# Performance work log

Hardware: AMD Instinct MI355X
Metric: run time of the kernel (lower is better)

The kernel has to match this reference:

```python
import jax, jax.numpy as jnp
import numpy as np

N_NODES = 100000
N_EDGES = 1600000
IN_CH = 128
HID = 32
N_GRAPHS = 64


def _gcn_conv(x, src, dst, W, b, n_nodes):
    # PyG GCNConv defaults: x' = D^{-1/2} (A + I) D^{-1/2} (x W) + b
    h = x @ W                                   # [N, out]
    loop = jnp.arange(n_nodes, dtype=src.dtype)
    s = jnp.concatenate([src, loop])            # add self-loops
    d = jnp.concatenate([dst, loop])
    deg = jax.ops.segment_sum(jnp.ones_like(d, dtype=h.dtype), d, num_segments=n_nodes)
    dinv = jnp.where(deg > 0, jax.lax.rsqrt(deg), 0.0)
    norm = dinv[s] * dinv[d]                    # [E+N]
    msg = h[s] * norm[:, None]                  # gather + scale
    out = jax.ops.segment_sum(msg, d, num_segments=n_nodes)  # scatter-add
    return out + b


def setup_inputs() -> dict:
    key = jax.random.key(0)
    ks = jax.random.split(key, 8)
    x = jax.random.normal(ks[0], (N_NODES, IN_CH), dtype=jnp.float32)
    edge_index = jax.random.randint(ks[1], (2, N_EDGES), 0, N_NODES, dtype=jnp.int32)
    batch = jnp.sort(jax.random.randint(ks[2], (N_NODES,), 0, N_GRAPHS, dtype=jnp.int32))
    W1 = jax.random.normal(ks[3], (IN_CH, HID), dtype=jnp.float32) * (1.0 / np.sqrt(IN_CH))
    b1 = jnp.zeros((HID,), dtype=jnp.float32)
    W2 = jax.random.normal(ks[4], (HID, HID), dtype=jnp.float32) * (1.0 / np.sqrt(HID))
    b2 = jnp.zeros((HID,), dtype=jnp.float32)
    Ws = jax.random.normal(ks[5], (HID, HID), dtype=jnp.float32) * (1.0 / np.sqrt(HID))
    bs = jnp.zeros((HID,), dtype=jnp.float32)
    return {"x": x, "edge_index": edge_index, "batch": batch,
            "W1": W1, "b1": b1, "W2": W2, "b2": b2, "Ws": Ws, "bs": bs}


def reference(x, edge_index, batch, W1, b1, W2, b2, Ws, bs):
    src, dst = edge_index[0], edge_index[1]
    n = x.shape[0]
    h = _gcn_conv(x, src, dst, W1, b1, n)
    h = jax.nn.relu(h)
    h = _gcn_conv(h, src, dst, W2, b2, n)       # [N, HID] node embeddings
    # global_mean_pool over graph ids
    ones = jnp.ones((n,), dtype=h.dtype)
    cnt = jax.ops.segment_sum(ones, batch, num_segments=N_GRAPHS)
    gsum = jax.ops.segment_sum(h, batch, num_segments=N_GRAPHS)
    g = gsum / jnp.maximum(cnt, 1.0)[:, None]   # [G, HID]
    summary = g @ Ws + bs
    return summary, h
```

## Files before the change

### kernel.cpp

```cpp
#include <hip/hip_runtime.h>

#define N_NODES  100000
#define N_EDGES  1600000
#define IN_CH    128
#define HID      32
#define N_GRAPHS 64

#define NBIN   391
#define CHUNK  4096
#define MGRID  391
#define STG    5120

#define OFF_B      0
#define OFF_EDGEPK 3200000
#define OFF_CSR    4800000
#define OFF_COLT   6400000
#define OFF_BINB   6400391
#define OFF_ROWPTR 6400784
#define OFF_DINV   6500785

__device__ __forceinline__ unsigned bfr(float f) {
    unsigned u = __float_as_uint(f);
    u += 0x7fffu + ((u >> 16) & 1u);
    return u >> 16;
}
__device__ __forceinline__ float bflo(unsigned w) { return __uint_as_float(w << 16); }
__device__ __forceinline__ float bfhi(unsigned w) { return __uint_as_float(w & 0xffff0000u); }

__global__ __launch_bounds__(512) void hist_kernel(const int* __restrict__ dst,
                                                   int* __restrict__ H) {
    __shared__ int s[512];
    int t = threadIdx.x, wg = blockIdx.x;
    s[t] = 0;
    __syncthreads();
    int e0 = wg * CHUNK, e1 = min(e0 + CHUNK, N_EDGES);
    for (int e = e0 + t; e < e1; e += 512) {
        int d = dst[e];
        if ((unsigned)d < N_NODES) atomicAdd(&s[d >> 8], 1);
    }
    __syncthreads();
    if (t < NBIN) H[t * MGRID + wg] = s[t];
}

__global__ __launch_bounds__(512) void scanrow_kernel(int* __restrict__ H,
                                                      int* __restrict__ colT) {
    __shared__ int s[512];
    int t = threadIdx.x, bin = blockIdx.x;
    s[t] = (t < MGRID) ? H[bin * MGRID + t] : 0;
    __syncthreads();
    for (int off = 1; off < 512; off <<= 1) {
        int v = (t >= off) ? s[t - off] : 0;
        __syncthreads();
        if (t >= off) s[t] += v;
        __syncthreads();
    }
    if (t < MGRID) H[bin * MGRID + t] = t ? s[t - 1] : 0;
    if (t == 0) colT[bin] = s[MGRID - 1];
}

__global__ __launch_bounds__(512) void scanbase_kernel(const int* __restrict__ colT,
                                                       int* __restrict__ binB,
                                                       int* __restrict__ row_ptr) {
    __shared__ int s[512];
    int t = threadIdx.x;
    s[t] = (t < NBIN) ? colT[t] : 0;
    __syncthreads();
    for (int off = 1; off < 512; off <<= 1) {
        int v = (t >= off) ? s[t - off] : 0;
        __syncthreads();
        if (t >= off) s[t] += v;
        __syncthreads();
    }
    if (t < NBIN) binB[t] = t ? s[t - 1] : 0;
    if (t == 0) { binB[NBIN] = s[NBIN - 1]; row_ptr[N_NODES] = s[NBIN - 1]; }
}

__global__ __launch_bounds__(512) void msplit_kernel(const int* __restrict__ src,
                                                     const int* __restrict__ dst,
                                                     const int* __restrict__ H,
                                                     const int* __restrict__ binB,
                                                     int* __restrict__ edgepk) {
    __shared__ int s[512];
    __shared__ int cur[NBIN];
    __shared__ int gb[NBIN];
    __shared__ int stage[CHUNK];
    __shared__ int gof[CHUNK];
    int t = threadIdx.x, wg = blockIdx.x;
    s[t] = 0;
    __syncthreads();
    int e0 = wg * CHUNK, e1 = min(e0 + CHUNK, N_EDGES);
    for (int e = e0 + t; e < e1; e += 512) {
        int d = dst[e];
        if ((unsigned)d < N_NODES) atomicAdd(&s[d >> 8], 1);
    }
    __syncthreads();
    for (int off = 1; off < 512; off <<= 1) {
        int v = (t >= off) ? s[t - off] : 0;
        __syncthreads();
        if (t >= off) s[t] += v;
        __syncthreads();
    }
    if (t < NBIN) {
        int lo = t ? s[t - 1] : 0;
        cur[t] = lo;
        gb[t] = binB[t] + H[t * MGRID + wg] - lo;
    }
    __syncthreads();
    for (int e = e0 + t; e < e1; e += 512) {
        int d = dst[e];
        if ((unsigned)d < N_NODES) {
            int b = d >> 8;
            int p = atomicAdd(&cur[b], 1);
            stage[p] = (src[e] << 8) | (d & 255);
            gof[p] = gb[b];
        }
    }
    __syncthreads();
    int total = s[511];
    for (int p = t; p < total; p += 512)
        edgepk[gof[p] + p] = stage[p];
}

__global__ __launch_bounds__(256) void csr2_kernel(const int* __restrict__ edgepk,
                                                   const int* __restrict__ binB,
                                                   int* __restrict__ row_ptr,
                                                   float* __restrict__ dinv,
                                                   int* __restrict__ csr) {
    __shared__ int cnt[256], s[256], cur[256];
    __shared__ int stage[STG];
    int t = threadIdx.x, bin = blockIdx.x;
    int ebase = binB[bin], eend = binB[bin + 1];
    int n = eend - ebase;
    cnt[t] = 0;
    __syncthreads();
    for (int p = ebase + t; p < eend; p += 256)
        atomicAdd(&cnt[edgepk[p] & 255], 1);
    __syncthreads();
    s[t] = cnt[t];
    __syncthreads();
    for (int off = 1; off < 256; off <<= 1) {
        int v = (t >= off) ? s[t - off] : 0;
        __syncthreads();
        if (t >= off) s[t] += v;
        __syncthreads();
    }
    int excl = t ? s[t - 1] : 0;
    int node = (bin << 8) + t;
    if (node < N_NODES) {
        dinv[node] = rsqrtf((float)(cnt[t] + 1));
        row_ptr[node] = ebase + excl;
    }
    cur[t] = excl;
    __syncthreads();
    for (int p = ebase + t; p < eend; p += 256) {
        int w = edgepk[p];
        int l = atomicAdd(&cur[w & 255], 1);
        int sv = w >> 8;
        if (l < STG) stage[l] = sv;
        else csr[ebase + l] = sv;
    }
    __syncthreads();
    int lim = min(n, STG);
    for (int l = t; l < lim; l += 256)
        csr[ebase + l] = stage[l];
}

#define XS1 132
__global__ __launch_bounds__(256) void gemm1_kernel(const float* __restrict__ x,
                                                    const float* __restrict__ W1,
                                                    const float* __restrict__ dinv,
                                                    unsigned* __restrict__ Bu) {
    __shared__ float Wl[IN_CH * HID];
    __shared__ float xs[32 * XS1];
    int tid = threadIdx.x;
    for (int j = tid; j < IN_CH * HID / 4; j += 256)
        ((float4*)Wl)[j] = ((const float4*)W1)[j];
    int row0 = blockIdx.x * 32;
    const float4* x4 = (const float4*)(x + (size_t)row0 * IN_CH);
    for (int j = tid; j < 32 * IN_CH / 4; j += 256) {
        int r = j >> 5, k4 = j & 31;
        ((float4*)&xs[r * XS1])[k4] = x4[j];
    }
    __syncthreads();
    int r = tid >> 3, cg = (tid & 7) * 4;
    const float* xr = &xs[r * XS1];
    float4 acc = {0.f, 0.f, 0.f, 0.f};
    #pragma unroll 8
    for (int k = 0; k < IN_CH; ++k) {
        float xv = xr[k];
        float4 w = *(const float4*)&Wl[k * HID + cg];
        acc.x += xv * w.x; acc.y += xv * w.y; acc.z += xv * w.z; acc.w += xv * w.w;
    }
    int row = row0 + r;
    float dv = dinv[row];
    uint2 p;
    p.x = bfr(acc.x * dv) | (bfr(acc.y * dv) << 16);
    p.y = bfr(acc.z * dv) | (bfr(acc.w * dv) << 16);
    *(uint2*)&Bu[(size_t)row * 16 + (tid & 7) * 2] = p;
}

#define XS2 36
__global__ __launch_bounds__(256) void gemm2_kernel(const float* __restrict__ in,
                                                    const float* __restrict__ W2,
                                                    const float* __restrict__ dinv,
                                                    unsigned* __restrict__ Bu) {
    __shared__ float Wl[HID * HID];
    __shared__ float xs[32 * XS2];
    int tid = threadIdx.x;
    ((float4*)Wl)[tid] = ((const float4*)W2)[tid];
    int row0 = blockIdx.x * 32;
    const float4* in4 = (const float4*)(in + (size_t)row0 * HID);
    {
        int r = tid >> 3, k4 = tid & 7;
        ((float4*)&xs[r * XS2])[k4] = in4[tid];
    }
    __syncthreads();
    int r = tid >> 3, cg = (tid & 7) * 4;
    const float* xr = &xs[r * XS2];
    float4 acc = {0.f, 0.f, 0.f, 0.f};
    #pragma unroll
    for (int k = 0; k < HID; ++k) {
        float xv = xr[k];
        float4 w = *(const float4*)&Wl[k * HID + cg];
        acc.x += xv * w.x; acc.y += xv * w.y; acc.z += xv * w.z; acc.w += xv * w.w;
    }
    int row = row0 + r;
    float dv = dinv[row];
    uint2 p;
    p.x = bfr(acc.x * dv) | (bfr(acc.y * dv) << 16);
    p.y = bfr(acc.z * dv) | (bfr(acc.w * dv) << 16);
    *(uint2*)&Bu[(size_t)row * 16 + (tid & 7) * 2] = p;
}

__global__ __launch_bounds__(256) void layer_kernel(const unsigned* __restrict__ Bu,
                                                    const int* __restrict__ csr,
                                                    const int* __restrict__ row_ptr,
                                                    const float* __restrict__ dinv,
                                                    const float* __restrict__ bias,
                                                    float* __restrict__ out,
                                                    int relu) {
    int tid = threadIdx.x;
    int node = blockIdx.x * 16 + (tid >> 4);
    int c2 = tid & 15;
    unsigned ws = Bu[(size_t)node * 16 + c2];
    float a0 = bflo(ws), a1 = bfhi(ws);
    int j = row_ptr[node], re = row_ptr[node + 1];
    for (; j + 8 <= re; j += 8) {
        int s0 = csr[j + 0], s1 = csr[j + 1], s2 = csr[j + 2], s3 = csr[j + 3];
        int s4 = csr[j + 4], s5 = csr[j + 5], s6 = csr[j + 6], s7 = csr[j + 7];
        unsigned w0 = Bu[(size_t)s0 * 16 + c2], w1 = Bu[(size_t)s1 * 16 + c2];
        unsigned w2 = Bu[(size_t)s2 * 16 + c2], w3 = Bu[(size_t)s3 * 16 + c2];
        unsigned w4 = Bu[(size_t)s4 * 16 + c2], w5 = Bu[(size_t)s5 * 16 + c2];
        unsigned w6 = Bu[(size_t)s6 * 16 + c2], w7 = Bu[(size_t)s7 * 16 + c2];
        a0 += ((bflo(w0) + bflo(w1)) + (bflo(w2) + bflo(w3)))
            + ((bflo(w4) + bflo(w5)) + (bflo(w6) + bflo(w7)));
        a1 += ((bfhi(w0) + bfhi(w1)) + (bfhi(w2) + bfhi(w3)))
            + ((bfhi(w4) + bfhi(w5)) + (bfhi(w6) + bfhi(w7)));
    }
    if (j + 4 <= re) {
        int s0 = csr[j], s1 = csr[j + 1], s2 = csr[j + 2], s3 = csr[j + 3];
        unsigned w0 = Bu[(size_t)s0 * 16 + c2], w1 = Bu[(size_t)s1 * 16 + c2];
        unsigned w2 = Bu[(size_t)s2 * 16 + c2], w3 = Bu[(size_t)s3 * 16 + c2];
        a0 += (bflo(w0) + bflo(w1)) + (bflo(w2) + bflo(w3));
        a1 += (bfhi(w0) + bfhi(w1)) + (bfhi(w2) + bfhi(w3));
        j += 4;
    }
    for (; j < re; ++j) {
        unsigned w = Bu[(size_t)csr[j] * 16 + c2];
        a0 += bflo(w); a1 += bfhi(w);
    }
    float dv = dinv[node];
    float2 o;
    o.x = a0 * dv + bias[2 * c2];
    o.y = a1 * dv + bias[2 * c2 + 1];
    if (relu) { o.x = fmaxf(o.x, 0.f); o.y = fmaxf(o.y, 0.f); }
    *(float2*)&out[(size_t)node * HID + 2 * c2] = o;
}

__global__ __launch_bounds__(256) void pool_kernel(const float* __restrict__ h,
                                                   const int* __restrict__ batch,
                                                   float* __restrict__ gsum,
                                                   float* __restrict__ cnt) {
    __shared__ float pool[N_GRAPHS * HID];
    __shared__ float cntl[N_GRAPHS];
    __shared__ int gmin, gmax;
    int t = threadIdx.x;
    for (int j = t; j < N_GRAPHS * HID; j += 256) pool[j] = 0.f;
    if (t < N_GRAPHS) cntl[t] = 0.f;
    if (t == 0) { gmin = N_GRAPHS; gmax = -1; }
    __syncthreads();
    int start = blockIdx.x * 256;
    int end = min(start + 256, N_NODES);
    int c = t & 31;
    float racc = 0.f;
    int rg = -1, rcnt = 0;
    for (int nb = start + (t >> 5); nb < end; nb += 8) {
        float v = h[(size_t)nb * HID + c];
        int g = batch[nb];
        if (g != rg) {
            if ((unsigned)rg < N_GRAPHS) {
                atomicAdd(&pool[rg * HID + c], racc);
                if (c == 0) {
                    atomicAdd(&cntl[rg], (float)rcnt);
                    atomicMin(&gmin, rg); atomicMax(&gmax, rg);
                }
            }
            rg = g; racc = v; rcnt = 1;
        } else { racc += v; ++rcnt; }
    }
    if ((unsigned)rg < N_GRAPHS) {
        atomicAdd(&pool[rg * HID + c], racc);
        if (c == 0) {
            atomicAdd(&cntl[rg], (float)rcnt);
            atomicMin(&gmin, rg); atomicMax(&gmax, rg);
        }
    }
    __syncthreads();
    int lo = gmin, hi = gmax;
    if (hi >= lo) {
        int span = (hi - lo + 1) * HID;
        for (int j = t; j < span; j += 256)
            atomicAdd(&gsum[lo * HID + j], pool[lo * HID + j]);
        for (int j = t; j <= hi - lo; j += 256)
            atomicAdd(&cnt[lo + j], cntl[lo + j]);
    }
}

__global__ void summary_kernel(const float* __restrict__ gsum, const float* __restrict__ cnt,
                               const float* __restrict__ Ws, const float* __restrict__ bs,
                               float* __restrict__ out) {
    int g = blockIdx.x, c = threadIdx.x;
    float inv = 1.f / fmaxf(cnt[g], 1.f);
    float acc = bs[c];
    #pragma unroll
    for (int k = 0; k < HID; ++k)
        acc += gsum[g * HID + k] * inv * Ws[k * HID + c];
    out[g * HID + c] = acc;
}

extern "C" void kernel_launch(void* const* d_in, const int* in_sizes, int n_in,
                              void* d_out, int out_size, void* d_ws, size_t ws_size,
                              hipStream_t stream) {
    const float* x    = (const float*)d_in[0];
    const int* edge   = (const int*)d_in[1];
    const int* src    = edge;
    const int* dst    = edge + N_EDGES;
    const int* batch  = (const int*)d_in[2];
    const float* W1   = (const float*)d_in[3];
    const float* b1   = (const float*)d_in[4];
    const float* W2   = (const float*)d_in[5];
    const float* b2   = (const float*)d_in[6];
    const float* Ws   = (const float*)d_in[7];
    const float* bs   = (const float*)d_in[8];

    float* ws      = (float*)d_ws;
    unsigned* Bu   = (unsigned*)(ws + OFF_B);
    int*   H       = (int*)(ws + OFF_B);
    int*   edgepk  = (int*)(ws + OFF_EDGEPK);
    int*   csr     = (int*)(ws + OFF_CSR);
    int*   colT    = (int*)(ws + OFF_COLT);
    int*   binB    = (int*)(ws + OFF_BINB);
    int*   row_ptr = (int*)(ws + OFF_ROWPTR);
    float* dinv    = ws + OFF_DINV;
    float* gsum    = ws + OFF_EDGEPK;
    float* cnt     = gsum + N_GRAPHS * HID;

    float* out     = (float*)d_out;
    float* out_sum = out;
    float* out_h   = out + N_GRAPHS * HID;

    hist_kernel    <<<MGRID, 512, 0, stream>>>(dst, H);
    scanrow_kernel <<<NBIN,  512, 0, stream>>>(H, colT);
    scanbase_kernel<<<1,     512, 0, stream>>>(colT, binB, row_ptr);
    msplit_kernel  <<<MGRID, 512, 0, stream>>>(src, dst, H, binB, edgepk);
    csr2_kernel    <<<NBIN,  256, 0, stream>>>(edgepk, binB, row_ptr, dinv, csr);

    gemm1_kernel<<<N_NODES / 32, 256, 0, stream>>>(x, W1, dinv, Bu);
    layer_kernel<<<N_NODES / 16, 256, 0, stream>>>(Bu, csr, row_ptr, dinv, b1, out_h, 1);

    gemm2_kernel<<<N_NODES / 32, 256, 0, stream>>>(out_h, W2, dinv, Bu);
    layer_kernel<<<N_NODES / 16, 256, 0, stream>>>(Bu, csr, row_ptr, dinv, b2, out_h, 0);

    hipMemsetAsync(gsum, 0, (N_GRAPHS * HID + N_GRAPHS) * sizeof(float), stream);
    pool_kernel<<<NBIN, 256, 0, stream>>>(out_h, batch, gsum, cnt);
    summary_kernel<<<N_GRAPHS, HID, 0, stream>>>(gsum, cnt, Ws, bs, out_sum);
}
```

Measured before the change: 240.2 us.

## Fuse layer-1 aggregation with W2 GEMM and layer-2 aggregation with mean pooling

The first aggregation kernel now applies bias and ReLU, stages each node's hidden row in shared memory, and multiplies by W2 in place. It writes the bf16 pre-scaled features for layer 2 directly, so the float hidden activations no longer go through global memory. The second aggregation kernel accumulates per-graph sums and counts into shared memory and flushes them with global atomics, which removes the separate pool pass over the output. In exchange there are more block-level syncs, many more small global atomic flushes (one per 16-node block), and a second bf16 buffer that reuses the edgepk workspace region.

```diff
diff --git a/kernel.cpp b/kernel.cpp
--- a/kernel.cpp
+++ b/kernel.cpp
@@ -18,6 +18,7 @@
 #define OFF_BINB   6400391
 #define OFF_ROWPTR 6400784
 #define OFF_DINV   6500785
+#define OFF_GS     6600800
 
 __device__ __forceinline__ unsigned bfr(float f) {
     unsigned u = __float_as_uint(f);
@@ -199,51 +200,21 @@
     *(uint2*)&Bu[(size_t)row * 16 + (tid & 7) * 2] = p;
 }
 
-#define XS2 36
-__global__ __launch_bounds__(256) void gemm2_kernel(const float* __restrict__ in,
-                                                    const float* __restrict__ W2,
-                                                    const float* __restrict__ dinv,
-                                                    unsigned* __restrict__ Bu) {
-    __shared__ float Wl[HID * HID];
-    __shared__ float xs[32 * XS2];
+__global__ __launch_bounds__(256) void layer1_fused_kernel(const unsigned* __restrict__ Bu,
+                                                           const int* __restrict__ csr,
+                                                           const int* __restrict__ row_ptr,
+                                                           const float* __restrict__ dinv,
+                                                           const float* __restrict__ bias,
+                                                           const float* __restrict__ W2,
+                                                           unsigned* __restrict__ Bu2) {
+    __shared__ float W2l[HID * HID];
+    __shared__ float hs[16 * 33];
     int tid = threadIdx.x;
-    ((float4*)Wl)[tid] = ((const float4*)W2)[tid];
-    int row0 = blockIdx.x * 32;
-    const float4* in4 = (const float4*)(in + (size_t)row0 * HID);
-    {
-        int r = tid >> 3, k4 = tid & 7;
-        ((float4*)&xs[r * XS2])[k4] = in4[tid];
-    }
-    __syncthreads();
-    int r = tid >> 3, cg = (tid & 7) * 4;
-    const float* xr = &xs[r * XS2];
-    float4 acc = {0.f, 0.f, 0.f, 0.f};
-    #pragma unroll
-    for (int k = 0; k < HID; ++k) {
-        float xv = xr[k];
-        float4 w = *(const float4*)&Wl[k * HID + cg];
-        acc.x += xv * w.x; acc.y += xv * w.y; acc.z += xv * w.z; acc.w += xv * w.w;
-    }
-    int row = row0 + r;
-    float dv = dinv[row];
-    uint2 p;
-    p.x = bfr(acc.x * dv) | (bfr(acc.y * dv) << 16);
-    p.y = bfr(acc.z * dv) | (bfr(acc.w * dv) << 16);
-    *(uint2*)&Bu[(size_t)row * 16 + (tid & 7) * 2] = p;
-}
-
-__global__ __launch_bounds__(256) void layer_kernel(const unsigned* __restrict__ Bu,
-                                                    const int* __restrict__ csr,
-                                                    const int* __restrict__ row_ptr,
-                                                    const float* __restrict__ dinv,
-                                                    const float* __restrict__ bias,
-                                                    float* __restrict__ out,
-                                                    int relu) {
-    int tid = threadIdx.x;
+    ((float4*)W2l)[tid] = ((const float4*)W2)[tid];
     int node = blockIdx.x * 16 + (tid >> 4);
     int c2 = tid & 15;
-    unsigned ws = Bu[(size_t)node * 16 + c2];
-    float a0 = bflo(ws), a1 = bfhi(ws);
+    unsigned ws0 = Bu[(size_t)node * 16 + c2];
+    float a0 = bflo(ws0), a1 = bfhi(ws0);
     int j = row_ptr[node], re = row_ptr[node + 1];
     for (; j + 8 <= re; j += 8) {
         int s0 = csr[j + 0], s1 = csr[j + 1], s2 = csr[j + 2], s3 = csr[j + 3];
@@ -270,60 +241,83 @@
         a0 += bflo(w); a1 += bfhi(w);
     }
     float dv = dinv[node];
+    float h0 = fmaxf(a0 * dv + bias[2 * c2], 0.f);
+    float h1 = fmaxf(a1 * dv + bias[2 * c2 + 1], 0.f);
+    int r = tid >> 4;
+    hs[r * 33 + 2 * c2]     = h0;
+    hs[r * 33 + 2 * c2 + 1] = h1;
+    __syncthreads();
+    const float* hr = &hs[r * 33];
+    float o0 = 0.f, o1 = 0.f;
+    #pragma unroll
+    for (int k = 0; k < HID; ++k) {
+        float hv = hr[k];
+        float2 w = *(const float2*)&W2l[k * HID + 2 * c2];
+        o0 += hv * w.x; o1 += hv * w.y;
+    }
+    Bu2[(size_t)node * 16 + c2] = bfr(o0 * dv) | (bfr(o1 * dv) << 16);
+}
+
+__global__ __launch_bounds__(256) void layer2_pool_kernel(const unsigned* __restrict__ Bu,
+                                                          const int* __restrict__ csr,
+                                                          const int* __restrict__ row_ptr,
+                                                          const float* __restrict__ dinv,
+                                                          const float* __restrict__ bias,
+                                                          const int* __restrict__ batch,
+                                                          float* __restrict__ out,
+                                                          float* __restrict__ gsum,
+                                                          float* __restrict__ cnt) {
+    __shared__ float pl[N_GRAPHS * HID];
+    __shared__ float pc[N_GRAPHS];
+    int tid = threadIdx.x;
+    int node0 = blockIdx.x * 16;
+    int g0 = batch[node0];
+    int span = batch[node0 + 15] - g0 + 1;
+    for (int q = tid; q < span * HID; q += 256) pl[q] = 0.f;
+    if (tid < span) pc[tid] = 0.f;
+    int node = node0 + (tid >> 4);
+    int c2 = tid & 15;
+    unsigned ws0 = Bu[(size_t)node * 16 + c2];
+    float a0 = bflo(ws0), a1 = bfhi(ws0);
+    int j = row_ptr[node], re = row_ptr[node + 1];
+    for (; j + 8 <= re; j += 8) {
+        int s0 = csr[j + 0], s1 = csr[j + 1], s2 = csr[j + 2], s3 = csr[j + 3];
+        int s4 = csr[j + 4], s5 = csr[j + 5], s6 = csr[j + 6], s7 = csr[j + 7];
+        unsigned w0 = Bu[(size_t)s0 * 16 + c2], w1 = Bu[(size_t)s1 * 16 + c2];
+        unsigned w2 = Bu[(size_t)s2 * 16 + c2], w3 = Bu[(size_t)s3 * 16 + c2];
+        unsigned w4 = Bu[(size_t)s4 * 16 + c2], w5 = Bu[(size_t)s5 * 16 + c2];
+        unsigned w6 = Bu[(size_t)s6 * 16 + c2], w7 = Bu[(size_t)s7 * 16 + c2];
+        a0 += ((bflo(w0) + bflo(w1)) + (bflo(w2) + bflo(w3)))
+            + ((bflo(w4) + bflo(w5)) + (bflo(w6) + bflo(w7)));
+        a1 += ((bfhi(w0) + bfhi(w1)) + (bfhi(w2) + bfhi(w3)))
+            + ((bfhi(w4) + bfhi(w5)) + (bfhi(w6) + bfhi(w7)));
+    }
+    if (j + 4 <= re) {
+        int s0 = csr[j], s1 = csr[j + 1], s2 = csr[j + 2], s3 = csr[j + 3];
+        unsigned w0 = Bu[(size_t)s0 * 16 + c2], w1 = Bu[(size_t)s1 * 16 + c2];
+        unsigned w2 = Bu[(size_t)s2 * 16 + c2], w3 = Bu[(size_t)s3 * 16 + c2];
+        a0 += (bflo(w0) + bflo(w1)) + (bflo(w2) + bflo(w3));
+        a1 += (bfhi(w0) + bfhi(w1)) + (bfhi(w2) + bfhi(w3));
+        j += 4;
+    }
+    for (; j < re; ++j) {
+        unsigned w = Bu[(size_t)csr[j] * 16 + c2];
+        a0 += bflo(w); a1 += bfhi(w);
+    }
+    float dv = dinv[node];
     float2 o;
     o.x = a0 * dv + bias[2 * c2];
     o.y = a1 * dv + bias[2 * c2 + 1];
-    if (relu) { o.x = fmaxf(o.x, 0.f); o.y = fmaxf(o.y, 0.f); }
     *(float2*)&out[(size_t)node * HID + 2 * c2] = o;
-}
-
-__global__ __launch_bounds__(256) void pool_kernel(const float* __restrict__ h,
-                                                   const int* __restrict__ batch,
-                                                   float* __restrict__ gsum,
-                                                   float* __restrict__ cnt) {
-    __shared__ float pool[N_GRAPHS * HID];
-    __shared__ float cntl[N_GRAPHS];
-    __shared__ int gmin, gmax;
-    int t = threadIdx.x;
-    for (int j = t; j < N_GRAPHS * HID; j += 256) pool[j] = 0.f;
-    if (t < N_GRAPHS) cntl[t] = 0.f;
-    if (t == 0) { gmin = N_GRAPHS; gmax = -1; }
-    __syncthreads();
-    int start = blockIdx.x * 256;
-    int end = min(start + 256, N_NODES);
-    int c = t & 31;
-    float racc = 0.f;
-    int rg = -1, rcnt = 0;
-    for (int nb = start + (t >> 5); nb < end; nb += 8) {
-        float v = h[(size_t)nb * HID + c];
-        int g = batch[nb];
-        if (g != rg) {
-            if ((unsigned)rg < N_GRAPHS) {
-                atomicAdd(&pool[rg * HID + c], racc);
-                if (c == 0) {
-                    atomicAdd(&cntl[rg], (float)rcnt);
-                    atomicMin(&gmin, rg); atomicMax(&gmax, rg);
-                }
-            }
-            rg = g; racc = v; rcnt = 1;
-        } else { racc += v; ++rcnt; }
-    }
-    if ((unsigned)rg < N_GRAPHS) {
-        atomicAdd(&pool[rg * HID + c], racc);
-        if (c == 0) {
-            atomicAdd(&cntl[rg], (float)rcnt);
-            atomicMin(&gmin, rg); atomicMax(&gmax, rg);
-        }
-    }
-    __syncthreads();
-    int lo = gmin, hi = gmax;
-    if (hi >= lo) {
-        int span = (hi - lo + 1) * HID;
-        for (int j = t; j < span; j += 256)
-            atomicAdd(&gsum[lo * HID + j], pool[lo * HID + j]);
-        for (int j = t; j <= hi - lo; j += 256)
-            atomicAdd(&cnt[lo + j], cntl[lo + j]);
-    }
+    int gl = batch[node] - g0;
+    __syncthreads();
+    atomicAdd(&pl[gl * HID + 2 * c2], o.x);
+    atomicAdd(&pl[gl * HID + 2 * c2 + 1], o.y);
+    if (c2 == 0) atomicAdd(&pc[gl], 1.f);
+    __syncthreads();
+    for (int q = tid; q < span * HID; q += 256)
+        atomicAdd(&gsum[g0 * HID + q], pl[q]);
+    if (tid < span) atomicAdd(&cnt[g0 + tid], pc[tid]);
 }
 
 __global__ void summary_kernel(const float* __restrict__ gsum, const float* __restrict__ cnt,
@@ -354,7 +348,8 @@
     const float* bs   = (const float*)d_in[8];
 
     float* ws      = (float*)d_ws;
-    unsigned* Bu   = (unsigned*)(ws + OFF_B);
+    unsigned* Bu1  = (unsigned*)(ws + OFF_B);
+    unsigned* Bu2  = (unsigned*)(ws + OFF_EDGEPK);
     int*   H       = (int*)(ws + OFF_B);
     int*   edgepk  = (int*)(ws + OFF_EDGEPK);
     int*   csr     = (int*)(ws + OFF_CSR);
@@ -362,7 +357,7 @@
     int*   binB    = (int*)(ws + OFF_BINB);
     int*   row_ptr = (int*)(ws + OFF_ROWPTR);
     float* dinv    = ws + OFF_DINV;
-    float* gsum    = ws + OFF_EDGEPK;
+    float* gsum    = ws + OFF_GS;
     float* cnt     = gsum + N_GRAPHS * HID;
 
     float* out     = (float*)d_out;
@@ -375,13 +370,11 @@
     msplit_kernel  <<<MGRID, 512, 0, stream>>>(src, dst, H, binB, edgepk);
     csr2_kernel    <<<NBIN,  256, 0, stream>>>(edgepk, binB, row_ptr, dinv, csr);
 
-    gemm1_kernel<<<N_NODES / 32, 256, 0, stream>>>(x, W1, dinv, Bu);
-    layer_kernel<<<N_NODES / 16, 256, 0, stream>>>(Bu, csr, row_ptr, dinv, b1, out_h, 1);
-
-    gemm2_kernel<<<N_NODES / 32, 256, 0, stream>>>(out_h, W2, dinv, Bu);
-    layer_kernel<<<N_NODES / 16, 256, 0, stream>>>(Bu, csr, row_ptr, dinv, b2, out_h, 0);
-
+    gemm1_kernel<<<N_NODES / 32, 256, 0, stream>>>(x, W1, dinv, Bu1);
     hipMemsetAsync(gsum, 0, (N_GRAPHS * HID + N_GRAPHS) * sizeof(float), stream);
-    pool_kernel<<<NBIN, 256, 0, stream>>>(out_h, batch, gsum, cnt);
+    layer1_fused_kernel<<<N_NODES / 16, 256, 0, stream>>>(Bu1, csr, row_ptr, dinv, b1, W2, Bu2);
+
+    layer2_pool_kernel<<<N_NODES / 16, 256, 0, stream>>>(Bu2, csr, row_ptr, dinv, b2, batch,
+                                                         out_h, gsum, cnt);
     summary_kernel<<<N_GRAPHS, HID, 0, stream>>>(gsum, cnt, Ws, bs, out_sum);
 }
```

Measured after the change: 267.1 us. +11.2%, slower.

## Split bf16 feature table into two column planes and gather each half separately

Applied to the files above, without the earlier changes.

The bf16 message table is stored as two 16-channel planes of 800k words each, and each layer's aggregation runs as two passes, one per plane. Each pass gathers 32-byte rows from a 3.2 MB plane instead of 64-byte rows from a 6.4 MB table, so the working set is more likely to stay cache-resident. CSR index loads and output stores become nontemporal, and the second layer's table moves to a separate workspace region. In exchange the CSR indices and row pointers are read twice per layer and there are two extra kernel launches.

```diff
diff --git a/kernel.cpp b/kernel.cpp
--- a/kernel.cpp
+++ b/kernel.cpp
@@ -10,6 +10,7 @@
 #define CHUNK  4096
 #define MGRID  391
 #define STG    5120
+#define PLN    800000
 
 #define OFF_B      0
 #define OFF_EDGEPK 3200000
@@ -18,6 +19,9 @@
 #define OFF_BINB   6400391
 #define OFF_ROWPTR 6400784
 #define OFF_DINV   6500785
+#define OFF_GS     6600800
+
+typedef float v2f __attribute__((ext_vector_type(2)));
 
 __device__ __forceinline__ unsigned bfr(float f) {
     unsigned u = __float_as_uint(f);
@@ -196,7 +200,8 @@
     uint2 p;
     p.x = bfr(acc.x * dv) | (bfr(acc.y * dv) << 16);
     p.y = bfr(acc.z * dv) | (bfr(acc.w * dv) << 16);
-    *(uint2*)&Bu[(size_t)row * 16 + (tid & 7) * 2] = p;
+    int c8 = tid & 7;
+    *(uint2*)(Bu + (size_t)(c8 >> 2) * PLN + (size_t)row * 8 + (c8 & 3) * 2) = p;
 }
 
 #define XS2 36
@@ -229,52 +234,62 @@
     uint2 p;
     p.x = bfr(acc.x * dv) | (bfr(acc.y * dv) << 16);
     p.y = bfr(acc.z * dv) | (bfr(acc.w * dv) << 16);
-    *(uint2*)&Bu[(size_t)row * 16 + (tid & 7) * 2] = p;
-}
-
-__global__ __launch_bounds__(256) void layer_kernel(const unsigned* __restrict__ Bu,
-                                                    const int* __restrict__ csr,
-                                                    const int* __restrict__ row_ptr,
-                                                    const float* __restrict__ dinv,
-                                                    const float* __restrict__ bias,
-                                                    float* __restrict__ out,
-                                                    int relu) {
+    int c8 = tid & 7;
+    *(uint2*)(Bu + (size_t)(c8 >> 2) * PLN + (size_t)row * 8 + (c8 & 3) * 2) = p;
+}
+
+__global__ __launch_bounds__(256) void gather_kernel(const unsigned* __restrict__ Bp,
+                                                     const int* __restrict__ csr,
+                                                     const int* __restrict__ row_ptr,
+                                                     const float* __restrict__ dinv,
+                                                     const float* __restrict__ bias,
+                                                     float* __restrict__ outp,
+                                                     int relu) {
     int tid = threadIdx.x;
-    int node = blockIdx.x * 16 + (tid >> 4);
-    int c2 = tid & 15;
-    unsigned ws = Bu[(size_t)node * 16 + c2];
-    float a0 = bflo(ws), a1 = bfhi(ws);
+    int node = blockIdx.x * 32 + (tid >> 3);
+    int c = tid & 7;
+    unsigned ws0 = Bp[(size_t)node * 8 + c];
+    float a0 = bflo(ws0), a1 = bfhi(ws0);
     int j = row_ptr[node], re = row_ptr[node + 1];
     for (; j + 8 <= re; j += 8) {
-        int s0 = csr[j + 0], s1 = csr[j + 1], s2 = csr[j + 2], s3 = csr[j + 3];
-        int s4 = csr[j + 4], s5 = csr[j + 5], s6 = csr[j + 6], s7 = csr[j + 7];
-        unsigned w0 = Bu[(size_t)s0 * 16 + c2], w1 = Bu[(size_t)s1 * 16 + c2];
-        unsigned w2 = Bu[(size_t)s2 * 16 + c2], w3 = Bu[(size_t)s3 * 16 + c2];
-        unsigned w4 = Bu[(size_t)s4 * 16 + c2], w5 = Bu[(size_t)s5 * 16 + c2];
-        unsigned w6 = Bu[(size_t)s6 * 16 + c2], w7 = Bu[(size_t)s7 * 16 + c2];
+        int s0 = __builtin_nontemporal_load(csr + j + 0);
+        int s1 = __builtin_nontemporal_load(csr + j + 1);
+        int s2 = __builtin_nontemporal_load(csr + j + 2);
+        int s3 = __builtin_nontemporal_load(csr + j + 3);
+        int s4 = __builtin_nontemporal_load(csr + j + 4);
+        int s5 = __builtin_nontemporal_load(csr + j + 5);
+        int s6 = __builtin_nontemporal_load(csr + j + 6);
+        int s7 = __builtin_nontemporal_load(csr + j + 7);
+        unsigned w0 = Bp[(size_t)s0 * 8 + c], w1 = Bp[(size_t)s1 * 8 + c];
+        unsigned w2 = Bp[(size_t)s2 * 8 + c], w3 = Bp[(size_t)s3 * 8 + c];
+        unsigned w4 = Bp[(size_t)s4 * 8 + c], w5 = Bp[(size_t)s5 * 8 + c];
+        unsigned w6 = Bp[(size_t)s6 * 8 + c], w7 = Bp[(size_t)s7 * 8 + c];
         a0 += ((bflo(w0) + bflo(w1)) + (bflo(w2) + bflo(w3)))
             + ((bflo(w4) + bflo(w5)) + (bflo(w6) + bflo(w7)));
         a1 += ((bfhi(w0) + bfhi(w1)) + (bfhi(w2) + bfhi(w3)))
             + ((bfhi(w4) + bfhi(w5)) + (bfhi(w6) + bfhi(w7)));
     }
     if (j + 4 <= re) {
-        int s0 = csr[j], s1 = csr[j + 1], s2 = csr[j + 2], s3 = csr[j + 3];
-        unsigned w0 = Bu[(size_t)s0 * 16 + c2], w1 = Bu[(size_t)s1 * 16 + c2];
-        unsigned w2 = Bu[(size_t)s2 * 16 + c2], w3 = Bu[(size_t)s3 * 16 + c2];
+        int s0 = __builtin_nontemporal_load(csr + j + 0);
+        int s1 = __builtin_nontemporal_load(csr + j + 1);
+        int s2 = __builtin_nontemporal_load(csr + j + 2);
+        int s3 = __builtin_nontemporal_load(csr + j + 3);
+        unsigned w0 = Bp[(size_t)s0 * 8 + c], w1 = Bp[(size_t)s1 * 8 + c];
+        unsigned w2 = Bp[(size_t)s2 * 8 + c], w3 = Bp[(size_t)s3 * 8 + c];
         a0 += (bflo(w0) + bflo(w1)) + (bflo(w2) + bflo(w3));
         a1 += (bfhi(w0) + bfhi(w1)) + (bfhi(w2) + bfhi(w3));
         j += 4;
     }
     for (; j < re; ++j) {
-        unsigned w = Bu[(size_t)csr[j] * 16 + c2];
+        unsigned w = Bp[(size_t)__builtin_nontemporal_load(csr + j) * 8 + c];
         a0 += bflo(w); a1 += bfhi(w);
     }
     float dv = dinv[node];
-    float2 o;
-    o.x = a0 * dv + bias[2 * c2];
-    o.y = a1 * dv + bias[2 * c2 + 1];
+    v2f o;
+    o.x = a0 * dv + bias[2 * c];
+    o.y = a1 * dv + bias[2 * c + 1];
     if (relu) { o.x = fmaxf(o.x, 0.f); o.y = fmaxf(o.y, 0.f); }
-    *(float2*)&out[(size_t)node * HID + 2 * c2] = o;
+    __builtin_nontemporal_store(o, (v2f*)(outp + (size_t)node * HID + 2 * c));
 }
 
 __global__ __launch_bounds__(256) void pool_kernel(const float* __restrict__ h,
@@ -354,7 +369,8 @@
     const float* bs   = (const float*)d_in[8];
 
     float* ws      = (float*)d_ws;
-    unsigned* Bu   = (unsigned*)(ws + OFF_B);
+    unsigned* Bu1  = (unsigned*)(ws + OFF_B);
+    unsigned* Bu2  = (unsigned*)(ws + OFF_EDGEPK);
     int*   H       = (int*)(ws + OFF_B);
     int*   edgepk  = (int*)(ws + OFF_EDGEPK);
     int*   csr     = (int*)(ws + OFF_CSR);
@@ -362,7 +378,7 @@
     int*   binB    = (int*)(ws + OFF_BINB);
     int*   row_ptr = (int*)(ws + OFF_ROWPTR);
     float* dinv    = ws + OFF_DINV;
-    float* gsum    = ws + OFF_EDGEPK;
+    float* gsum    = ws + OFF_GS;
     float* cnt     = gsum + N_GRAPHS * HID;
 
     float* out     = (float*)d_out;
@@ -375,11 +391,13 @@
     msplit_kernel  <<<MGRID, 512, 0, stream>>>(src, dst, H, binB, edgepk);
     csr2_kernel    <<<NBIN,  256, 0, stream>>>(edgepk, binB, row_ptr, dinv, csr);
 
-    gemm1_kernel<<<N_NODES / 32, 256, 0, stream>>>(x, W1, dinv, Bu);
-    layer_kernel<<<N_NODES / 16, 256, 0, stream>>>(Bu, csr, row_ptr, dinv, b1, out_h, 1);
-
-    gemm2_kernel<<<N_NODES / 32, 256, 0, stream>>>(out_h, W2, dinv, Bu);
-    layer_kernel<<<N_NODES / 16, 256, 0, stream>>>(Bu, csr, row_ptr, dinv, b2, out_h, 0);
+    gemm1_kernel<<<N_NODES / 32, 256, 0, stream>>>(x, W1, dinv, Bu1);
+    gather_kernel<<<N_NODES / 32, 256, 0, stream>>>(Bu1,       csr, row_ptr, dinv, b1,      out_h,      1);
+    gather_kernel<<<N_NODES / 32, 256, 0, stream>>>(Bu1 + PLN, csr, row_ptr, dinv, b1 + 16, out_h + 16, 1);
+
+    gemm2_kernel<<<N_NODES / 32, 256, 0, stream>>>(out_h, W2, dinv, Bu2);
+    gather_kernel<<<N_NODES / 32, 256, 0, stream>>>(Bu2,       csr, row_ptr, dinv, b2,      out_h,      0);
+    gather_kernel<<<N_NODES / 32, 256, 0, stream>>>(Bu2 + PLN, csr, row_ptr, dinv, b2 + 16, out_h + 16, 0);
 
     hipMemsetAsync(gsum, 0, (N_GRAPHS * HID + N_GRAPHS) * sizeof(float), stream);
     pool_kernel<<<NBIN, 256, 0, stream>>>(out_h, batch, gsum, cnt);
```

Measured after the change: 275.6 us. 14.7% more time.

## Balance edge aggregation across threads with LDS atomic accumulation per node group

Applied to the files above, without the earlier changes.

The CSR build now packs each edge's local destination index into the top byte alongside the source id. The aggregation kernel splits a block's contiguous 32-node edge range evenly across 16 thread groups and accumulates into shared memory with atomics, then adds the self-loop term, scales, and writes float4 outputs. The aim is to remove load imbalance from varying node degrees, at the cost of many LDS atomic adds per edge. Packing 24-bit source ids limits the node count to 2^24.

```diff
diff --git a/kernel.cpp b/kernel.cpp
--- a/kernel.cpp
+++ b/kernel.cpp
@@ -10,6 +10,7 @@
 #define CHUNK  4096
 #define MGRID  391
 #define STG    5120
+#define GN     32
 
 #define OFF_B      0
 #define OFF_EDGEPK 3200000
@@ -154,10 +155,11 @@
     __syncthreads();
     for (int p = ebase + t; p < eend; p += 256) {
         int w = edgepk[p];
-        int l = atomicAdd(&cur[w & 255], 1);
-        int sv = w >> 8;
-        if (l < STG) stage[l] = sv;
-        else csr[ebase + l] = sv;
+        int dl = w & 255;
+        int l = atomicAdd(&cur[dl], 1);
+        int pk = (int)(((unsigned)dl << 24) | (unsigned)(w >> 8));
+        if (l < STG) stage[l] = pk;
+        else csr[ebase + l] = pk;
     }
     __syncthreads();
     int lim = min(n, STG);
@@ -232,49 +234,83 @@
     *(uint2*)&Bu[(size_t)row * 16 + (tid & 7) * 2] = p;
 }
 
-__global__ __launch_bounds__(256) void layer_kernel(const unsigned* __restrict__ Bu,
-                                                    const int* __restrict__ csr,
-                                                    const int* __restrict__ row_ptr,
-                                                    const float* __restrict__ dinv,
-                                                    const float* __restrict__ bias,
-                                                    float* __restrict__ out,
-                                                    int relu) {
+#define AS 33
+__global__ __launch_bounds__(256) void gather_acc_kernel(const unsigned* __restrict__ Bu,
+                                                         const int* __restrict__ csr,
+                                                         const int* __restrict__ row_ptr,
+                                                         const float* __restrict__ dinv,
+                                                         const float* __restrict__ bias,
+                                                         float* __restrict__ out,
+                                                         int relu) {
+    __shared__ float acc[GN * AS];
     int tid = threadIdx.x;
-    int node = blockIdx.x * 16 + (tid >> 4);
-    int c2 = tid & 15;
-    unsigned ws = Bu[(size_t)node * 16 + c2];
-    float a0 = bflo(ws), a1 = bfhi(ws);
-    int j = row_ptr[node], re = row_ptr[node + 1];
-    for (; j + 8 <= re; j += 8) {
-        int s0 = csr[j + 0], s1 = csr[j + 1], s2 = csr[j + 2], s3 = csr[j + 3];
-        int s4 = csr[j + 4], s5 = csr[j + 5], s6 = csr[j + 6], s7 = csr[j + 7];
-        unsigned w0 = Bu[(size_t)s0 * 16 + c2], w1 = Bu[(size_t)s1 * 16 + c2];
-        unsigned w2 = Bu[(size_t)s2 * 16 + c2], w3 = Bu[(size_t)s3 * 16 + c2];
-        unsigned w4 = Bu[(size_t)s4 * 16 + c2], w5 = Bu[(size_t)s5 * 16 + c2];
-        unsigned w6 = Bu[(size_t)s6 * 16 + c2], w7 = Bu[(size_t)s7 * 16 + c2];
-        a0 += ((bflo(w0) + bflo(w1)) + (bflo(w2) + bflo(w3)))
-            + ((bflo(w4) + bflo(w5)) + (bflo(w6) + bflo(w7)));
-        a1 += ((bfhi(w0) + bfhi(w1)) + (bfhi(w2) + bfhi(w3)))
-            + ((bfhi(w4) + bfhi(w5)) + (bfhi(w6) + bfhi(w7)));
-    }
-    if (j + 4 <= re) {
-        int s0 = csr[j], s1 = csr[j + 1], s2 = csr[j + 2], s3 = csr[j + 3];
-        unsigned w0 = Bu[(size_t)s0 * 16 + c2], w1 = Bu[(size_t)s1 * 16 + c2];
-        unsigned w2 = Bu[(size_t)s2 * 16 + c2], w3 = Bu[(size_t)s3 * 16 + c2];
-        a0 += (bflo(w0) + bflo(w1)) + (bflo(w2) + bflo(w3));
-        a1 += (bfhi(w0) + bfhi(w1)) + (bfhi(w2) + bfhi(w3));
-        j += 4;
-    }
-    for (; j < re; ++j) {
-        unsigned w = Bu[(size_t)csr[j] * 16 + c2];
-        a0 += bflo(w); a1 += bfhi(w);
-    }
+    int n0 = blockIdx.x * GN;
+    for (int q = tid; q < GN * AS; q += 256) acc[q] = 0.f;
+    int j0 = row_ptr[n0], j1 = row_ptr[n0 + GN];
+    __syncthreads();
+    int g = tid >> 4, c2 = tid & 15;
+    int lbase = n0 & 255;
+    int nE = j1 - j0;
+    int epg = (nE + 15) >> 4;
+    int e = j0 + g * epg;
+    int ee = min(e + epg, j1);
+    for (; e + 8 <= ee; e += 8) {
+        unsigned u0 = (unsigned)csr[e + 0], u1 = (unsigned)csr[e + 1];
+        unsigned u2 = (unsigned)csr[e + 2], u3 = (unsigned)csr[e + 3];
+        unsigned u4 = (unsigned)csr[e + 4], u5 = (unsigned)csr[e + 5];
+        unsigned u6 = (unsigned)csr[e + 6], u7 = (unsigned)csr[e + 7];
+        unsigned w0 = Bu[(size_t)(u0 & 0xFFFFFFu) * 16 + c2];
+        unsigned w1 = Bu[(size_t)(u1 & 0xFFFFFFu) * 16 + c2];
+        unsigned w2 = Bu[(size_t)(u2 & 0xFFFFFFu) * 16 + c2];
+        unsigned w3 = Bu[(size_t)(u3 & 0xFFFFFFu) * 16 + c2];
+        unsigned w4 = Bu[(size_t)(u4 & 0xFFFFFFu) * 16 + c2];
+        unsigned w5 = Bu[(size_t)(u5 & 0xFFFFFFu) * 16 + c2];
+        unsigned w6 = Bu[(size_t)(u6 & 0xFFFFFFu) * 16 + c2];
+        unsigned w7 = Bu[(size_t)(u7 & 0xFFFFFFu) * 16 + c2];
+        int d0 = (int)(u0 >> 24) - lbase, d1 = (int)(u1 >> 24) - lbase;
+        int d2 = (int)(u2 >> 24) - lbase, d3 = (int)(u3 >> 24) - lbase;
+        int d4 = (int)(u4 >> 24) - lbase, d5 = (int)(u5 >> 24) - lbase;
+        int d6 = (int)(u6 >> 24) - lbase, d7 = (int)(u7 >> 24) - lbase;
+        atomicAdd(&acc[d0 * AS + 2 * c2],     bflo(w0));
+        atomicAdd(&acc[d0 * AS + 2 * c2 + 1], bfhi(w0));
+        atomicAdd(&acc[d1 * AS + 2 * c2],     bflo(w1));
+        atomicAdd(&acc[d1 * AS + 2 * c2 + 1], bfhi(w1));
+        atomicAdd(&acc[d2 * AS + 2 * c2],     bflo(w2));
+        atomicAdd(&acc[d2 * AS + 2 * c2 + 1], bfhi(w2));
+        atomicAdd(&acc[d3 * AS + 2 * c2],     bflo(w3));
+        atomicAdd(&acc[d3 * AS + 2 * c2 + 1], bfhi(w3));
+        atomicAdd(&acc[d4 * AS + 2 * c2],     bflo(w4));
+        atomicAdd(&acc[d4 * AS + 2 * c2 + 1], bfhi(w4));
+        atomicAdd(&acc[d5 * AS + 2 * c2],     bflo(w5));
+        atomicAdd(&acc[d5 * AS + 2 * c2 + 1], bfhi(w5));
+        atomicAdd(&acc[d6 * AS + 2 * c2],     bflo(w6));
+        atomicAdd(&acc[d6 * AS + 2 * c2 + 1], bfhi(w6));
+        atomicAdd(&acc[d7 * AS + 2 * c2],     bflo(w7));
+        atomicAdd(&acc[d7 * AS + 2 * c2 + 1], bfhi(w7));
+    }
+    for (; e < ee; ++e) {
+        unsigned u = (unsigned)csr[e];
+        unsigned w = Bu[(size_t)(u & 0xFFFFFFu) * 16 + c2];
+        int d = (int)(u >> 24) - lbase;
+        atomicAdd(&acc[d * AS + 2 * c2],     bflo(w));
+        atomicAdd(&acc[d * AS + 2 * c2 + 1], bfhi(w));
+    }
+    __syncthreads();
+    int i = tid >> 3, c4 = (tid & 7) * 4;
+    int node = n0 + i;
+    uint2 sw = *(const uint2*)&Bu[(size_t)node * 16 + (c4 >> 1)];
     float dv = dinv[node];
-    float2 o;
-    o.x = a0 * dv + bias[2 * c2];
-    o.y = a1 * dv + bias[2 * c2 + 1];
-    if (relu) { o.x = fmaxf(o.x, 0.f); o.y = fmaxf(o.y, 0.f); }
-    *(float2*)&out[(size_t)node * HID + 2 * c2] = o;
+    const float* ar = &acc[i * AS + c4];
+    float4 o;
+    o.x = (ar[0] + bflo(sw.x)) * dv + bias[c4 + 0];
+    o.y = (ar[1] + bfhi(sw.x)) * dv + bias[c4 + 1];
+    o.z = (ar[2] + bflo(sw.y)) * dv + bias[c4 + 2];
+    o.w = (ar[3] + bfhi(sw.y)) * dv + bias[c4 + 3];
+    if (relu) {
+        o.x = fmaxf(o.x, 0.f); o.y = fmaxf(o.y, 0.f);
+        o.z = fmaxf(o.z, 0.f); o.w = fmaxf(o.w, 0.f);
+    }
+    *(float4*)&out[(size_t)node * HID + c4] = o;
 }
 
 __global__ __launch_bounds__(256) void pool_kernel(const float* __restrict__ h,
@@ -376,10 +412,10 @@
     csr2_kernel    <<<NBIN,  256, 0, stream>>>(edgepk, binB, row_ptr, dinv, csr);
 
     gemm1_kernel<<<N_NODES / 32, 256, 0, stream>>>(x, W1, dinv, Bu);
-    layer_kernel<<<N_NODES / 16, 256, 0, stream>>>(Bu, csr, row_ptr, dinv, b1, out_h, 1);
+    gather_acc_kernel<<<N_NODES / GN, 256, 0, stream>>>(Bu, csr, row_ptr, dinv, b1, out_h, 1);
 
     gemm2_kernel<<<N_NODES / 32, 256, 0, stream>>>(out_h, W2, dinv, Bu);
-    layer_kernel<<<N_NODES / 16, 256, 0, stream>>>(Bu, csr, row_ptr, dinv, b2, out_h, 0);
+    gather_acc_kernel<<<N_NODES / GN, 256, 0, stream>>>(Bu, csr, row_ptr, dinv, b2, out_h, 0);
 
     hipMemsetAsync(gsum, 0, (N_GRAPHS * HID + N_GRAPHS) * sizeof(float), stream);
     pool_kernel<<<NBIN, 256, 0, stream>>>(out_h, batch, gsum, cnt);
```

Result: slower. 736.3 us (+206.6%).
